# Kernel optimization log

Measured on AMD Instinct MI355X. Metric: run time of the kernel, lower is better.

Reference implementation:

```python
import jax, jax.numpy as jnp
import numpy as np

N, M, D = 1024, 1024, 512


def setup_inputs() -> dict:
    key = jax.random.key(0)
    ks = jax.random.split(key, 12)
    s = 1.0 / np.sqrt(D)
    return {
        "q": jax.random.normal(ks[0], (N, D), jnp.float32),
        "k": jax.random.normal(ks[1], (M, D), jnp.float32),
        "v": jax.random.normal(ks[2], (M, D), jnp.float32),
        "mask": jax.random.randint(ks[3], (N, M), 0, 2) > 0,
        "Wq": jax.random.normal(ks[4], (D, D), jnp.float32) * s,
        "bq": jax.random.normal(ks[5], (D,), jnp.float32) * s,
        "Wk": jax.random.normal(ks[6], (D, D), jnp.float32) * s,
        "bk": jax.random.normal(ks[7], (D,), jnp.float32) * s,
        "Wv": jax.random.normal(ks[8], (D, D), jnp.float32) * s,
        "bv": jax.random.normal(ks[9], (D,), jnp.float32) * s,
        "Ww": jax.random.normal(ks[10], (D,), jnp.float32) * s,
        "bw": jax.random.normal(ks[11], (1,), jnp.float32) * s,
    }


def reference(q, k, v, mask, Wq, bq, Wk, bk, Wv, bv, Ww, bw):
    # Linear projections (torch Linear: x @ W.T + b)
    qp = q @ Wq.T + bq  # [N, D]
    kp = k @ Wk.T + bk  # [M, D]
    vp = v @ Wv.T + bv  # [M, D]
    # Bahdanau additive score: W(tanh(q_n + k_m)) -> [N, M]
    h = jnp.tanh(qp[:, None, :] + kp[None, :, :])  # [N, M, D]
    scores = jnp.einsum('nmd,d->nm', h, Ww) + bw[0]
    scores = jnp.where(mask, scores, jnp.float32(-1000000.0))
    attn = jax.nn.softmax(scores, axis=1)  # softmax over M (dim 1)
    context = jnp.einsum('nm,md->nd', attn, vp)  # [N, D]
    return context
```

## Files before the change

kernel.cpp:

```cpp
#include <hip/hip_runtime.h>
#include <hip/hip_bf16.h>
#include <float.h>


#define NROWS 1024
#define DDIM  512
#define MDIM  1024

__device__ __forceinline__ void load_lds16(const float* g, float* l) {
    __builtin_amdgcn_global_load_lds(
        (const __attribute__((address_space(1))) void*)g,
        (__attribute__((address_space(3))) void*)l, 16, 0, 0);
}

__global__ __launch_bounds__(256) void proj_gemm(
    const float* __restrict__ q, const float* __restrict__ kk_,
    const float* __restrict__ v,
    const float* __restrict__ Wq, const float* __restrict__ bq,
    const float* __restrict__ Wk, const float* __restrict__ bk,
    const float* __restrict__ Wv, const float* __restrict__ bv,
    float* __restrict__ eqT, float* __restrict__ ek, float* __restrict__ vp,
    float* __restrict__ rsum, float* __restrict__ outz, float CS)
{
    __shared__ __align__(16) float As[4096];
    __shared__ __align__(16) float Bs[4096];

    const float* A; const float* B; const float* bias; float* out;
    int C, expo, biasRow;
    if (blockIdx.z == 0)      { A = Wq;  B = q;  bias = bq; out = eqT; C = 1024; expo = 1; biasRow = 1; }
    else if (blockIdx.z == 1) { A = kk_; B = Wk; bias = bk; out = ek;  C = 512;  expo = 1; biasRow = 0; }
    else                      { A = v;   B = Wv; bias = bv; out = vp;  C = 512;  expo = 0; biasRow = 0; }

    const int bi = (blockIdx.z == 0) ? blockIdx.y : blockIdx.x;
    const int bj = (blockIdx.z == 0) ? blockIdx.x : blockIdx.y;

    const int t  = threadIdx.x;
    const int tx = t & 15;
    const int ty = t >> 4;
    const int i0 = bi * 64;
    const int j0 = bj * 64;

    if (blockIdx.z == 0) {
        const int jb = blockIdx.y * 16 + blockIdx.x;
        float4 zz = {0.f, 0.f, 0.f, 0.f};
#pragma unroll
        for (int p = 0; p < 4; ++p)
            *(float4*)&outz[(size_t)jb * 4096 + (t + p * 256) * 4] = zz;
        if (jb == 0) *(float4*)&rsum[t * 4] = zz;
    }

    float acc[4][4] = {};
    float4 pa[4], pb[4];

#pragma unroll
    for (int p = 0; p < 4; ++p) {
        int idx = t + p * 256;
        int r = idx >> 4, c4 = idx & 15;
        pa[p] = *(const float4*)&A[(size_t)(i0 + r) * DDIM + c4 * 4];
        pb[p] = *(const float4*)&B[(size_t)(j0 + r) * DDIM + c4 * 4];
    }

    for (int kc = 0; kc < 8; ++kc) {
        __syncthreads();
#pragma unroll
        for (int p = 0; p < 4; ++p) {
            int idx = t + p * 256;
            int r = idx >> 4, c4 = idx & 15;
            int base = (c4 * 4) * 64 + (((r >> 2) ^ c4) << 2) + (r & 3);
            As[base]       = pa[p].x;  As[base + 64]  = pa[p].y;
            As[base + 128] = pa[p].z;  As[base + 192] = pa[p].w;
            Bs[base]       = pb[p].x;  Bs[base + 64]  = pb[p].y;
            Bs[base + 128] = pb[p].z;  Bs[base + 192] = pb[p].w;
        }
        __syncthreads();
        if (kc < 7) {
            const int k0 = (kc + 1) * 64;
#pragma unroll
            for (int p = 0; p < 4; ++p) {
                int idx = t + p * 256;
                int r = idx >> 4, c4 = idx & 15;
                pa[p] = *(const float4*)&A[(size_t)(i0 + r) * DDIM + k0 + c4 * 4];
                pb[p] = *(const float4*)&B[(size_t)(j0 + r) * DDIM + k0 + c4 * 4];
            }
        }
#pragma unroll
        for (int kg = 0; kg < 16; ++kg) {
            const int ao = ((ty ^ kg) << 2);
            const int bo = ((tx ^ kg) << 2);
#pragma unroll
            for (int kq = 0; kq < 4; ++kq) {
                int kk = kg * 4 + kq;
                float4 a = *(const float4*)&As[kk * 64 + ao];
                float4 b = *(const float4*)&Bs[kk * 64 + bo];
                float av4[4] = {a.x, a.y, a.z, a.w};
                float bv4[4] = {b.x, b.y, b.z, b.w};
#pragma unroll
                for (int i = 0; i < 4; ++i)
#pragma unroll
                    for (int j = 0; j < 4; ++j)
                        acc[i][j] = fmaf(av4[i], bv4[j], acc[i][j]);
            }
        }
    }

    const float CLAMP = 8192.0f;
#pragma unroll
    for (int i = 0; i < 4; ++i) {
        int row = i0 + ty * 4 + i;
        float ov[4];
#pragma unroll
        for (int j = 0; j < 4; ++j) {
            float bval = biasRow ? bias[row] : bias[j0 + tx * 4 + j];
            float val = acc[i][j] + bval;
            ov[j] = expo ? fminf(__builtin_amdgcn_exp2f(val * CS), CLAMP) : val;
        }
        float4 o = {ov[0], ov[1], ov[2], ov[3]};
        *(float4*)&out[(size_t)row * C + j0 + tx * 4] = o;
    }
}

#define DCH  32
#define SNCH 128
__global__ __launch_bounds__(256) void score_kernel(const float* __restrict__ eqT,
                                                    const float* __restrict__ ek,
                                                    const float* __restrict__ Ww,
                                                    const int* __restrict__ mask,
                                                    float* __restrict__ PT,
                                                    float* __restrict__ rsum)
{
    __shared__ __align__(16) float ks[DCH * SNCH];
    __shared__ __align__(16) float es[16 * DCH];
    __shared__ __align__(16) float wws[DCH];
    const int t    = threadIdx.x;
    const int lane = t & 63;
    const int w    = t >> 6;
    const int n0   = blockIdx.x * SNCH;
    const int m0   = blockIdx.y * 16;

    float acc[4][2] = {};

    for (int d0 = 0; d0 < DDIM; d0 += DCH) {
        __syncthreads();
#pragma unroll
        for (int i = 0; i < 4; ++i) {
            int r2 = w * 8 + i * 2;
            const float* g = eqT + (size_t)(d0 + r2 + (lane >> 5)) * NROWS
                             + n0 + (lane & 31) * 4;
            load_lds16(g, &ks[r2 * SNCH]);
        }
#pragma unroll
        for (int p = 0; p < 2; ++p) {
            int idx = t + p * 256;
            int ml = idx >> 5, dd = idx & 31;
            es[ml * DCH + dd] = ek[(size_t)(m0 + ml) * DDIM + d0 + dd];
        }
        if (t < DCH) wws[t] = Ww[d0 + t];
        __syncthreads();

#pragma unroll
        for (int dq = 0; dq < DCH; dq += 4) {
            float2 k0 = *(const float2*)&ks[(dq + 0) * SNCH + lane * 2];
            float2 k1 = *(const float2*)&ks[(dq + 1) * SNCH + lane * 2];
            float2 k2 = *(const float2*)&ks[(dq + 2) * SNCH + lane * 2];
            float2 k3 = *(const float2*)&ks[(dq + 3) * SNCH + lane * 2];
            float4 wg = *(const float4*)&wws[dq];
#pragma unroll
            for (int mm = 0; mm < 4; ++mm) {
                float4 eg = *(const float4*)&es[(w * 4 + mm) * DCH + dq];
#pragma unroll
                for (int j = 0; j < 2; ++j) {
                    float A0 = fmaf(j ? k0.y : k0.x, eg.x, 1.0f);
                    float A1 = fmaf(j ? k1.y : k1.x, eg.y, 1.0f);
                    float A2 = fmaf(j ? k2.y : k2.x, eg.z, 1.0f);
                    float A3 = fmaf(j ? k3.y : k3.x, eg.w, 1.0f);
                    float n01 = fmaf(wg.y, A0, wg.x * A1);
                    float d01 = A0 * A1;
                    float n23 = fmaf(wg.w, A2, wg.z * A3);
                    float d23 = A2 * A3;
                    float num = fmaf(n01, d23, n23 * d01);
                    float den = d01 * d23;
                    acc[mm][j] = fmaf(num, __builtin_amdgcn_rcpf(den), acc[mm][j]);
                }
            }
        }
    }

    const float C2 = -2.8853900817779268f;
    const int n = n0 + lane * 2;
    float rs0 = 0.f, rs1 = 0.f;
#pragma unroll
    for (int mm = 0; mm < 4; ++mm) {
        int m = m0 + w * 4 + mm;
        int mk0 = mask[(size_t)n * MDIM + m];
        int mk1 = mask[(size_t)(n + 1) * MDIM + m];
        float2 o;
        o.x = mk0 ? __builtin_amdgcn_exp2f(acc[mm][0] * C2) : 0.f;
        o.y = mk1 ? __builtin_amdgcn_exp2f(acc[mm][1] * C2) : 0.f;
        rs0 += o.x; rs1 += o.y;
        *(float2*)&PT[(size_t)m * NROWS + n] = o;
    }

    __syncthreads();
    ks[w * SNCH + lane * 2]     = rs0;
    ks[w * SNCH + lane * 2 + 1] = rs1;
    __syncthreads();
    if (t < SNCH) {
        float tot = (ks[t] + ks[SNCH + t]) + (ks[2 * SNCH + t] + ks[3 * SNCH + t]);
        atomicAdd(&rsum[n0 + t], tot);
    }
}

__global__ __launch_bounds__(256) void ctx_gemm(const float* __restrict__ PT,
                                                const float* __restrict__ vp,
                                                const float* __restrict__ rsum,
                                                float* __restrict__ out)
{
    __shared__ __align__(16) float pts[64 * 68];
    __shared__ __align__(16) float vs[64 * 68];
    const int t  = threadIdx.x;
    const int tx = t & 15;
    const int ty = t >> 4;
    const int d0 = blockIdx.x * 64;
    const int n0 = blockIdx.y * 64;
    const int mb = blockIdx.z * 512;

    float acc[4][4] = {};

    for (int m0 = mb; m0 < mb + 512; m0 += 64) {
        __syncthreads();
#pragma unroll
        for (int p = 0; p < 4; ++p) {
            int idx = t + p * 256;
            int r = idx >> 4, c4 = idx & 15;
            *(float4*)&pts[r * 68 + c4 * 4] =
                *(const float4*)&PT[(size_t)(m0 + r) * NROWS + n0 + c4 * 4];
            *(float4*)&vs[r * 68 + c4 * 4] =
                *(const float4*)&vp[(size_t)(m0 + r) * DDIM + d0 + c4 * 4];
        }
        __syncthreads();
#pragma unroll 8
        for (int mm = 0; mm < 64; ++mm) {
            float4 a = *(const float4*)&pts[mm * 68 + ty * 4];
            float4 b = *(const float4*)&vs[mm * 68 + tx * 4];
            float av4[4] = {a.x, a.y, a.z, a.w};
            float bv4[4] = {b.x, b.y, b.z, b.w};
#pragma unroll
            for (int i = 0; i < 4; ++i)
#pragma unroll
                for (int j = 0; j < 4; ++j)
                    acc[i][j] = fmaf(av4[i], bv4[j], acc[i][j]);
        }
    }

#pragma unroll
    for (int i = 0; i < 4; ++i) {
        int nrow = n0 + ty * 4 + i;
        float inv = __builtin_amdgcn_rcpf(rsum[nrow]);
#pragma unroll
        for (int j = 0; j < 4; ++j)
            atomicAdd(&out[(size_t)nrow * DDIM + d0 + tx * 4 + j], acc[i][j] * inv);
    }
}

extern "C" void kernel_launch(void* const* d_in, const int* in_sizes, int n_in,
                              void* d_out, int out_size, void* d_ws, size_t ws_size,
                              hipStream_t stream)
{
    const float* q    = (const float*)d_in[0];
    const float* k    = (const float*)d_in[1];
    const float* v    = (const float*)d_in[2];
    const int*   mask = (const int*)d_in[3];
    const float* Wq   = (const float*)d_in[4];
    const float* bq   = (const float*)d_in[5];
    const float* Wk   = (const float*)d_in[6];
    const float* bk   = (const float*)d_in[7];
    const float* Wv   = (const float*)d_in[8];
    const float* bv   = (const float*)d_in[9];
    const float* Ww   = (const float*)d_in[10];

    float* ws   = (float*)d_ws;
    float* eqT  = ws;
    float* ek   = ws + 524288;
    float* vp   = ws + 1048576;
    float* PT   = ws + 1572864;
    float* rsum = ws + 2621440;
    float* out  = (float*)d_out;

    const float CS = 2.8853900817779268f;

    proj_gemm<<<dim3(16, 8, 3), dim3(256), 0, stream>>>(q, k, v, Wq, bq, Wk, bk,
                                                        Wv, bv, eqT, ek, vp,
                                                        rsum, out, CS);
    score_kernel<<<dim3(8, 64), dim3(256), 0, stream>>>(eqT, ek, Ww, mask, PT, rsum);
    ctx_gemm<<<dim3(8, 16, 2), dim3(256), 0, stream>>>(PT, vp, rsum, out);
}
```

Measured before the change: 199.4 us.

## Use split-bf16 MFMA for projection and context GEMMs, drop atomics

```diff
diff --git a/kernel.cpp b/kernel.cpp
--- a/kernel.cpp
+++ b/kernel.cpp
@@ -6,6 +6,18 @@
 #define NROWS 1024
 #define DDIM  512
 #define MDIM  1024
+
+typedef __attribute__((ext_vector_type(8))) short s8v;
+typedef __attribute__((ext_vector_type(4))) float f4v;
+
+__device__ __forceinline__ ushort f2bf(float f) {
+    unsigned u = __float_as_uint(f);
+    u = u + 0x7FFFu + ((u >> 16) & 1u);
+    return (ushort)(u >> 16);
+}
+__device__ __forceinline__ float bf2f(ushort h) {
+    return __uint_as_float(((unsigned)h) << 16);
+}
 
 __device__ __forceinline__ void load_lds16(const float* g, float* l) {
     __builtin_amdgcn_global_load_lds(
@@ -19,103 +31,129 @@
     const float* __restrict__ Wq, const float* __restrict__ bq,
     const float* __restrict__ Wk, const float* __restrict__ bk,
     const float* __restrict__ Wv, const float* __restrict__ bv,
-    float* __restrict__ eqT, float* __restrict__ ek, float* __restrict__ vp,
-    float* __restrict__ rsum, float* __restrict__ outz, float CS)
+    float* __restrict__ eqT, float* __restrict__ ek,
+    ushort* __restrict__ vph, ushort* __restrict__ vpl,
+    float* __restrict__ rsum, float CS)
 {
-    __shared__ __align__(16) float As[4096];
-    __shared__ __align__(16) float Bs[4096];
-
-    const float* A; const float* B; const float* bias; float* out;
-    int C, expo, biasRow;
-    if (blockIdx.z == 0)      { A = Wq;  B = q;  bias = bq; out = eqT; C = 1024; expo = 1; biasRow = 1; }
-    else if (blockIdx.z == 1) { A = kk_; B = Wk; bias = bk; out = ek;  C = 512;  expo = 1; biasRow = 0; }
-    else                      { A = v;   B = Wv; bias = bv; out = vp;  C = 512;  expo = 0; biasRow = 0; }
-
-    const int bi = (blockIdx.z == 0) ? blockIdx.y : blockIdx.x;
-    const int bj = (blockIdx.z == 0) ? blockIdx.x : blockIdx.y;
-
-    const int t  = threadIdx.x;
-    const int tx = t & 15;
-    const int ty = t >> 4;
-    const int i0 = bi * 64;
-    const int j0 = bj * 64;
-
-    if (blockIdx.z == 0) {
-        const int jb = blockIdx.y * 16 + blockIdx.x;
+    __shared__ ushort Ah[4096], Al[4096], Bh[4096], Bl[4096];
+
+    const float* A; const float* B; const float* bias;
+    int biasRow;
+    if (blockIdx.z == 0)      { A = Wq;  B = q;   bias = bq; biasRow = 1; }
+    else if (blockIdx.z == 1) { A = kk_; B = Wk;  bias = bk; biasRow = 0; }
+    else                      { A = Wv;  B = v;   bias = bv; biasRow = 1; }
+
+    const int bi = (blockIdx.z == 1) ? blockIdx.x : blockIdx.y;
+    const int bj = (blockIdx.z == 1) ? blockIdx.y : blockIdx.x;
+
+    const int t    = threadIdx.x;
+    const int lane = t & 63;
+    const int w    = t >> 6;
+    const int lm   = lane & 15;
+    const int lq   = lane >> 4;
+    const int i0   = bi * 64;
+    const int j0   = bj * 64;
+    const int mh   = (w >> 1) * 32;
+    const int nh   = (w & 1) * 32;
+
+    if (blockIdx.z == 0 && bi == 0 && bj == 0) {
         float4 zz = {0.f, 0.f, 0.f, 0.f};
-#pragma unroll
-        for (int p = 0; p < 4; ++p)
-            *(float4*)&outz[(size_t)jb * 4096 + (t + p * 256) * 4] = zz;
-        if (jb == 0) *(float4*)&rsum[t * 4] = zz;
-    }
-
-    float acc[4][4] = {};
+        *(float4*)&rsum[t * 4] = zz;
+    }
+
+    f4v acc[2][2] = {{{0.f,0.f,0.f,0.f},{0.f,0.f,0.f,0.f}},
+                     {{0.f,0.f,0.f,0.f},{0.f,0.f,0.f,0.f}}};
     float4 pa[4], pb[4];
 
+    const int sr = t >> 4, sc4 = t & 15;
 #pragma unroll
     for (int p = 0; p < 4; ++p) {
-        int idx = t + p * 256;
-        int r = idx >> 4, c4 = idx & 15;
-        pa[p] = *(const float4*)&A[(size_t)(i0 + r) * DDIM + c4 * 4];
-        pb[p] = *(const float4*)&B[(size_t)(j0 + r) * DDIM + c4 * 4];
+        int r = sr + p * 16;
+        pa[p] = *(const float4*)&A[(size_t)(i0 + r) * DDIM + sc4 * 4];
+        pb[p] = *(const float4*)&B[(size_t)(j0 + r) * DDIM + sc4 * 4];
     }
 
     for (int kc = 0; kc < 8; ++kc) {
         __syncthreads();
 #pragma unroll
         for (int p = 0; p < 4; ++p) {
-            int idx = t + p * 256;
-            int r = idx >> 4, c4 = idx & 15;
-            int base = (c4 * 4) * 64 + (((r >> 2) ^ c4) << 2) + (r & 3);
-            As[base]       = pa[p].x;  As[base + 64]  = pa[p].y;
-            As[base + 128] = pa[p].z;  As[base + 192] = pa[p].w;
-            Bs[base]       = pb[p].x;  Bs[base + 64]  = pb[p].y;
-            Bs[base + 128] = pb[p].z;  Bs[base + 192] = pb[p].w;
+            int r = sr + p * 16;
+            int ad = r * 64 + (((sc4 >> 1) ^ (r & 7)) << 3) + (sc4 & 1) * 4;
+            float af[4] = {pa[p].x, pa[p].y, pa[p].z, pa[p].w};
+            float bf[4] = {pb[p].x, pb[p].y, pb[p].z, pb[p].w};
+            ushort ah4[4], al4[4], bh4[4], bl4[4];
+#pragma unroll
+            for (int e = 0; e < 4; ++e) {
+                ah4[e] = f2bf(af[e]); al4[e] = f2bf(af[e] - bf2f(ah4[e]));
+                bh4[e] = f2bf(bf[e]); bl4[e] = f2bf(bf[e] - bf2f(bh4[e]));
+            }
+            *(ushort4*)&Ah[ad] = *(ushort4*)ah4;
+            *(ushort4*)&Al[ad] = *(ushort4*)al4;
+            *(ushort4*)&Bh[ad] = *(ushort4*)bh4;
+            *(ushort4*)&Bl[ad] = *(ushort4*)bl4;
         }
         __syncthreads();
         if (kc < 7) {
             const int k0 = (kc + 1) * 64;
 #pragma unroll
             for (int p = 0; p < 4; ++p) {
-                int idx = t + p * 256;
-                int r = idx >> 4, c4 = idx & 15;
-                pa[p] = *(const float4*)&A[(size_t)(i0 + r) * DDIM + k0 + c4 * 4];
-                pb[p] = *(const float4*)&B[(size_t)(j0 + r) * DDIM + k0 + c4 * 4];
-            }
-        }
-#pragma unroll
-        for (int kg = 0; kg < 16; ++kg) {
-            const int ao = ((ty ^ kg) << 2);
-            const int bo = ((tx ^ kg) << 2);
-#pragma unroll
-            for (int kq = 0; kq < 4; ++kq) {
-                int kk = kg * 4 + kq;
-                float4 a = *(const float4*)&As[kk * 64 + ao];
-                float4 b = *(const float4*)&Bs[kk * 64 + bo];
-                float av4[4] = {a.x, a.y, a.z, a.w};
-                float bv4[4] = {b.x, b.y, b.z, b.w};
-#pragma unroll
-                for (int i = 0; i < 4; ++i)
-#pragma unroll
-                    for (int j = 0; j < 4; ++j)
-                        acc[i][j] = fmaf(av4[i], bv4[j], acc[i][j]);
-            }
+                int r = sr + p * 16;
+                pa[p] = *(const float4*)&A[(size_t)(i0 + r) * DDIM + k0 + sc4 * 4];
+                pb[p] = *(const float4*)&B[(size_t)(j0 + r) * DDIM + k0 + sc4 * 4];
+            }
+        }
+#pragma unroll
+        for (int ks = 0; ks < 2; ++ks) {
+            const int kb = ks * 4 + lq;
+            s8v afh[2], afl[2], bfh[2], bfl[2];
+#pragma unroll
+            for (int g = 0; g < 2; ++g) {
+                int ra = mh + g * 16 + lm;
+                int rb = nh + g * 16 + lm;
+                int aa = ra * 64 + ((kb ^ (ra & 7)) << 3);
+                int ab = rb * 64 + ((kb ^ (rb & 7)) << 3);
+                afh[g] = *(const s8v*)&Ah[aa];
+                afl[g] = *(const s8v*)&Al[aa];
+                bfh[g] = *(const s8v*)&Bh[ab];
+                bfl[g] = *(const s8v*)&Bl[ab];
+            }
+#pragma unroll
+            for (int mi = 0; mi < 2; ++mi)
+#pragma unroll
+                for (int ni = 0; ni < 2; ++ni) {
+                    acc[mi][ni] = __builtin_amdgcn_mfma_f32_16x16x32_bf16(
+                        afh[mi], bfh[ni], acc[mi][ni], 0, 0, 0);
+                    acc[mi][ni] = __builtin_amdgcn_mfma_f32_16x16x32_bf16(
+                        afh[mi], bfl[ni], acc[mi][ni], 0, 0, 0);
+                    acc[mi][ni] = __builtin_amdgcn_mfma_f32_16x16x32_bf16(
+                        afl[mi], bfh[ni], acc[mi][ni], 0, 0, 0);
+                }
         }
     }
 
     const float CLAMP = 8192.0f;
 #pragma unroll
-    for (int i = 0; i < 4; ++i) {
-        int row = i0 + ty * 4 + i;
-        float ov[4];
-#pragma unroll
-        for (int j = 0; j < 4; ++j) {
-            float bval = biasRow ? bias[row] : bias[j0 + tx * 4 + j];
-            float val = acc[i][j] + bval;
-            ov[j] = expo ? fminf(__builtin_amdgcn_exp2f(val * CS), CLAMP) : val;
-        }
-        float4 o = {ov[0], ov[1], ov[2], ov[3]};
-        *(float4*)&out[(size_t)row * C + j0 + tx * 4] = o;
+    for (int mi = 0; mi < 2; ++mi) {
+#pragma unroll
+        for (int ni = 0; ni < 2; ++ni) {
+#pragma unroll
+            for (int p = 0; p < 4; ++p) {
+                int row = i0 + mh + mi * 16 + lq * 4 + p;
+                int col = j0 + nh + ni * 16 + lm;
+                float val = acc[mi][ni][p] + (biasRow ? bias[row] : bias[col]);
+                if (blockIdx.z == 0) {
+                    eqT[(size_t)row * 1024 + col] =
+                        fminf(__builtin_amdgcn_exp2f(val * CS), CLAMP);
+                } else if (blockIdx.z == 1) {
+                    ek[(size_t)row * 512 + col] =
+                        fminf(__builtin_amdgcn_exp2f(val * CS), CLAMP);
+                } else {
+                    ushort h = f2bf(val);
+                    vph[(size_t)row * 1024 + col] = h;
+                    vpl[(size_t)row * 1024 + col] = f2bf(val - bf2f(h));
+                }
+            }
+        }
     }
 }
 
@@ -125,7 +163,8 @@
                                                     const float* __restrict__ ek,
                                                     const float* __restrict__ Ww,
                                                     const int* __restrict__ mask,
-                                                    float* __restrict__ PT,
+                                                    ushort* __restrict__ Ph,
+                                                    ushort* __restrict__ Pl,
                                                     float* __restrict__ rsum)
 {
     __shared__ __align__(16) float ks[DCH * SNCH];
@@ -188,16 +227,25 @@
     const float C2 = -2.8853900817779268f;
     const int n = n0 + lane * 2;
     float rs0 = 0.f, rs1 = 0.f;
+    ushort h0[4], l0[4], h1[4], l1[4];
 #pragma unroll
     for (int mm = 0; mm < 4; ++mm) {
         int m = m0 + w * 4 + mm;
         int mk0 = mask[(size_t)n * MDIM + m];
         int mk1 = mask[(size_t)(n + 1) * MDIM + m];
-        float2 o;
-        o.x = mk0 ? __builtin_amdgcn_exp2f(acc[mm][0] * C2) : 0.f;
-        o.y = mk1 ? __builtin_amdgcn_exp2f(acc[mm][1] * C2) : 0.f;
-        rs0 += o.x; rs1 += o.y;
-        *(float2*)&PT[(size_t)m * NROWS + n] = o;
+        float o0 = mk0 ? __builtin_amdgcn_exp2f(acc[mm][0] * C2) : 0.f;
+        float o1 = mk1 ? __builtin_amdgcn_exp2f(acc[mm][1] * C2) : 0.f;
+        rs0 += o0; rs1 += o1;
+        h0[mm] = f2bf(o0); l0[mm] = f2bf(o0 - bf2f(h0[mm]));
+        h1[mm] = f2bf(o1); l1[mm] = f2bf(o1 - bf2f(h1[mm]));
+    }
+    {
+        size_t b0 = (size_t)n * MDIM + m0 + w * 4;
+        size_t b1 = (size_t)(n + 1) * MDIM + m0 + w * 4;
+        *(ushort4*)&Ph[b0] = *(ushort4*)h0;
+        *(ushort4*)&Pl[b0] = *(ushort4*)l0;
+        *(ushort4*)&Ph[b1] = *(ushort4*)h1;
+        *(ushort4*)&Pl[b1] = *(ushort4*)l1;
     }
 
     __syncthreads();
@@ -210,55 +258,43 @@
     }
 }
 
-__global__ __launch_bounds__(256) void ctx_gemm(const float* __restrict__ PT,
-                                                const float* __restrict__ vp,
+__global__ __launch_bounds__(256) void ctx_gemm(const ushort* __restrict__ Ph,
+                                                const ushort* __restrict__ Pl,
+                                                const ushort* __restrict__ vph,
+                                                const ushort* __restrict__ vpl,
                                                 const float* __restrict__ rsum,
                                                 float* __restrict__ out)
 {
-    __shared__ __align__(16) float pts[64 * 68];
-    __shared__ __align__(16) float vs[64 * 68];
-    const int t  = threadIdx.x;
-    const int tx = t & 15;
-    const int ty = t >> 4;
-    const int d0 = blockIdx.x * 64;
-    const int n0 = blockIdx.y * 64;
-    const int mb = blockIdx.z * 512;
-
-    float acc[4][4] = {};
-
-    for (int m0 = mb; m0 < mb + 512; m0 += 64) {
-        __syncthreads();
-#pragma unroll
-        for (int p = 0; p < 4; ++p) {
-            int idx = t + p * 256;
-            int r = idx >> 4, c4 = idx & 15;
-            *(float4*)&pts[r * 68 + c4 * 4] =
-                *(const float4*)&PT[(size_t)(m0 + r) * NROWS + n0 + c4 * 4];
-            *(float4*)&vs[r * 68 + c4 * 4] =
-                *(const float4*)&vp[(size_t)(m0 + r) * DDIM + d0 + c4 * 4];
-        }
-        __syncthreads();
-#pragma unroll 8
-        for (int mm = 0; mm < 64; ++mm) {
-            float4 a = *(const float4*)&pts[mm * 68 + ty * 4];
-            float4 b = *(const float4*)&vs[mm * 68 + tx * 4];
-            float av4[4] = {a.x, a.y, a.z, a.w};
-            float bv4[4] = {b.x, b.y, b.z, b.w};
-#pragma unroll
-            for (int i = 0; i < 4; ++i)
-#pragma unroll
-                for (int j = 0; j < 4; ++j)
-                    acc[i][j] = fmaf(av4[i], bv4[j], acc[i][j]);
-        }
-    }
-
-#pragma unroll
-    for (int i = 0; i < 4; ++i) {
-        int nrow = n0 + ty * 4 + i;
+    const int t    = threadIdx.x;
+    const int lane = t & 63;
+    const int w    = t >> 6;
+    const int lm   = lane & 15;
+    const int lq   = lane >> 4;
+    const int d0   = blockIdx.x * 64 + w * 16;
+    const int n0   = blockIdx.y * 16;
+
+    const ushort* pAh = Ph  + (size_t)(n0 + lm) * MDIM + lq * 8;
+    const ushort* pAl = Pl  + (size_t)(n0 + lm) * MDIM + lq * 8;
+    const ushort* pBh = vph + (size_t)(d0 + lm) * MDIM + lq * 8;
+    const ushort* pBl = vpl + (size_t)(d0 + lm) * MDIM + lq * 8;
+
+    f4v acc = {0.f, 0.f, 0.f, 0.f};
+#pragma unroll 4
+    for (int m0 = 0; m0 < MDIM; m0 += 32) {
+        s8v ah = *(const s8v*)(pAh + m0);
+        s8v al = *(const s8v*)(pAl + m0);
+        s8v bh = *(const s8v*)(pBh + m0);
+        s8v bl = *(const s8v*)(pBl + m0);
+        acc = __builtin_amdgcn_mfma_f32_16x16x32_bf16(ah, bh, acc, 0, 0, 0);
+        acc = __builtin_amdgcn_mfma_f32_16x16x32_bf16(ah, bl, acc, 0, 0, 0);
+        acc = __builtin_amdgcn_mfma_f32_16x16x32_bf16(al, bh, acc, 0, 0, 0);
+    }
+
+#pragma unroll
+    for (int p = 0; p < 4; ++p) {
+        int nrow = n0 + lq * 4 + p;
         float inv = __builtin_amdgcn_rcpf(rsum[nrow]);
-#pragma unroll
-        for (int j = 0; j < 4; ++j)
-            atomicAdd(&out[(size_t)nrow * DDIM + d0 + tx * 4 + j], acc[i][j] * inv);
+        out[(size_t)nrow * DDIM + d0 + lm] = acc[p] * inv;
     }
 }
 
@@ -278,19 +314,22 @@
     const float* bv   = (const float*)d_in[9];
     const float* Ww   = (const float*)d_in[10];
 
-    float* ws   = (float*)d_ws;
-    float* eqT  = ws;
-    float* ek   = ws + 524288;
-    float* vp   = ws + 1048576;
-    float* PT   = ws + 1572864;
-    float* rsum = ws + 2621440;
-    float* out  = (float*)d_out;
+    float* ws    = (float*)d_ws;
+    float* eqT   = ws;
+    float* ek    = ws + 524288;
+    ushort* vph  = (ushort*)(ws + 1048576);
+    ushort* vpl  = (ushort*)(ws + 1310720);
+    ushort* Ph   = (ushort*)(ws + 1572864);
+    ushort* Pl   = (ushort*)(ws + 2097152);
+    float* rsum  = ws + 2621440;
+    float* out   = (float*)d_out;
 
     const float CS = 2.8853900817779268f;
 
     proj_gemm<<<dim3(16, 8, 3), dim3(256), 0, stream>>>(q, k, v, Wq, bq, Wk, bk,
-                                                        Wv, bv, eqT, ek, vp,
-                                                        rsum, out, CS);
-    score_kernel<<<dim3(8, 64), dim3(256), 0, stream>>>(eqT, ek, Ww, mask, PT, rsum);
-    ctx_gemm<<<dim3(8, 16, 2), dim3(256), 0, stream>>>(PT, vp, rsum, out);
-}
+                                                        Wv, bv, eqT, ek,
+                                                        vph, vpl, rsum, CS);
+    score_kernel<<<dim3(8, 64), dim3(256), 0, stream>>>(eqT, ek, Ww, mask,
+                                                        Ph, Pl, rsum);
+    ctx_gemm<<<dim3(8, 64), dim3(256), 0, stream>>>(Ph, Pl, vph, vpl, rsum, out);
+}
```

After: 181.7 us. -8.9%, faster.
